# Performance work log

Hardware: AMD Instinct MI355X
Metric: run time of the kernel (lower is better)

The kernel has to match this reference:

```python
import jax, jax.numpy as jnp
import numpy as np

# dims: L layers, T steps, N envs, D d_model, H heads, DH d_head, M mem_len, DI d_inner
L, T, N, D, H, DH, M, DI = 6, 128, 32, 1024, 16, 64, 128, 4096


def _layer_norm(x, g, b, eps=1e-5):
    mu = jnp.mean(x, axis=-1, keepdims=True)
    var = jnp.mean(jnp.square(x - mu), axis=-1, keepdims=True)
    return (x - mu) * jax.lax.rsqrt(var + eps) * g + b


def _rel_shift(x):
    # x: (n, h, q, k) with k axis indexed by relative distance (k-1 .. 0)
    n, h, q, k = x.shape
    x = jnp.pad(x, ((0, 0), (0, 0), (0, 0), (1, 0)))
    x = x.reshape(n, h, k + 1, q)[:, :, 1:, :].reshape(n, h, q, k)
    return x


def setup_inputs() -> dict:
    key = jax.random.key(0)
    ks = jax.random.split(key, 16)
    s = 0.02
    inp = {
        "x": jax.random.normal(ks[0], (T * N, D), jnp.float32),
        "context": jax.random.normal(ks[1], (T * N, D), jnp.float32),
        "mems": jax.random.normal(ks[2], (L, N, M, D), jnp.float32),
        "masks": jnp.ones((T * N,), jnp.float32),
        "Wq": jax.random.normal(ks[3], (L, D, H * DH), jnp.float32) * s,
        "Wk": jax.random.normal(ks[4], (L, D, H * DH), jnp.float32) * s,
        "Wv": jax.random.normal(ks[5], (L, D, H * DH), jnp.float32) * s,
        "Wr": jax.random.normal(ks[6], (L, D, H * DH), jnp.float32) * s,
        "Wo": jax.random.normal(ks[7], (L, H * DH, D), jnp.float32) * s,
        "W1": jax.random.normal(ks[8], (L, D, DI), jnp.float32) * s,
        "b1": jnp.zeros((L, DI), jnp.float32),
        "W2": jax.random.normal(ks[9], (L, DI, D), jnp.float32) * s,
        "b2": jnp.zeros((L, D), jnp.float32),
        "ln1_g": jnp.ones((L, D), jnp.float32),
        "ln1_b": jnp.zeros((L, D), jnp.float32),
        "ln2_g": jnp.ones((L, D), jnp.float32),
        "ln2_b": jnp.zeros((L, D), jnp.float32),
        "r_w_bias": jax.random.normal(ks[10], (H, DH), jnp.float32) * s,
        "r_r_bias": jax.random.normal(ks[11], (H, DH), jnp.float32) * s,
    }
    return inp


def reference(x, context, mems, masks, Wq, Wk, Wv, Wr, Wo, W1, b1, W2, b2,
              ln1_g, ln1_b, ln2_g, ln2_b, r_w_bias, r_r_bias):
    n = mems.shape[1]
    t = x.shape[0] // n
    m = mems.shape[2]
    klen = m + t
    dh = r_w_bias.shape[-1]
    h_heads = r_w_bias.shape[0]

    xs = x.reshape(t, n, -1)
    ctx = context.reshape(t, n, -1)
    mk = masks.reshape(t, n)

    # zero memories for envs that reset at the first step (mems * masks)
    mems = mems * mk[0][None, :, None, None]

    # episode-reset attention mask: token i attends token j iff j<=i and no
    # reset (mask==0) happened between them; memory visible only before any reset
    ep = jnp.cumsum((mk == 0.0).astype(jnp.int32), axis=0)  # (t, n)
    epT = ep.T  # (n, t)
    causal = jnp.tril(jnp.ones((t, t), bool))
    allow_seq = causal[None, :, :] & (epT[:, :, None] == epT[:, None, :])  # (n,t,t)
    allow_mem = jnp.broadcast_to((epT == 0)[:, :, None], (n, t, m))  # (n,t,m)
    allow = jnp.concatenate([allow_mem, allow_seq], axis=-1)[:, None]  # (n,1,t,K)

    # sinusoidal relative position embedding, distances klen-1 .. 0
    pos = jnp.arange(klen - 1, -1, -1, dtype=x.dtype)
    inv_freq = 1.0 / (10000.0 ** (jnp.arange(0, xs.shape[-1], 2, dtype=x.dtype) / xs.shape[-1]))
    ang = pos[:, None] * inv_freq[None, :]
    R = jnp.concatenate([jnp.sin(ang), jnp.cos(ang)], axis=-1)  # (K, D)

    h = xs + ctx  # fuse observation features with goal context
    scale = 1.0 / jnp.sqrt(jnp.asarray(dh, x.dtype))

    n_layer = mems.shape[0]
    for l in range(n_layer):
        cat = jnp.concatenate([jnp.transpose(mems[l], (1, 0, 2)), h], axis=0)  # (K,n,D)
        q = (h @ Wq[l]).reshape(t, n, h_heads, dh)
        k = (cat @ Wk[l]).reshape(klen, n, h_heads, dh)
        v = (cat @ Wv[l]).reshape(klen, n, h_heads, dh)
        r = (R @ Wr[l]).reshape(klen, h_heads, dh)
        AC = jnp.einsum('inhd,jnhd->nhij', q + r_w_bias, k)
        BD = _rel_shift(jnp.einsum('inhd,jhd->nhij', q + r_r_bias, r))
        score = (AC + BD) * scale
        score = jnp.where(allow, score, -1e9)
        attn = jax.nn.softmax(score, axis=-1)
        o = jnp.einsum('nhij,jnhd->inhd', attn, v).reshape(t, n, h_heads * dh) @ Wo[l]
        h = _layer_norm(h + o, ln1_g[l], ln1_b[l])
        f = jax.nn.relu(h @ W1[l] + b1[l]) @ W2[l] + b2[l]
        h = _layer_norm(h + f, ln2_g[l], ln2_b[l])

    return h.reshape(t * n, -1)
```

## Files before the change

### kernel.cpp

```cpp
#include <hip/hip_runtime.h>
#include <stdint.h>

#define DEV static __device__ __forceinline__

typedef __attribute__((ext_vector_type(4))) float f32x4;
typedef __attribute__((ext_vector_type(8))) short bf16x8;
typedef __attribute__((ext_vector_type(4))) short s16x4;

static constexpr int L_ = 6, T_ = 128, NE = 32, D_ = 1024, H_ = 16, DH_ = 64, M_ = 128, DI_ = 4096;
static constexpr int KLEN = M_ + T_;
static constexpr int TN = T_ * NE;
static constexpr int NB = NE * H_;

DEV unsigned short f2bf(float f) {
  unsigned u = __builtin_bit_cast(unsigned, f);
  u += 0x7FFFu + ((u >> 16) & 1u);
  return (unsigned short)(u >> 16);
}
DEV float bf2f(unsigned short h) {
  unsigned u = ((unsigned)h) << 16;
  return __builtin_bit_cast(float, u);
}

DEV void gload16(const unsigned short* g, unsigned short* lds) {
  __builtin_amdgcn_global_load_lds(
      (const __attribute__((address_space(1))) unsigned int*)g,
      (__attribute__((address_space(3))) unsigned int*)lds, 16, 0, 0);
}

#define WAITV0 asm volatile("s_waitcnt vmcnt(0)" ::: "memory")

DEV void stage128(const unsigned short* __restrict__ Ab, int lda,
                  const unsigned short* __restrict__ Bb, int ldb,
                  unsigned short* lA, unsigned short* lB,
                  int m0, int n0, int k0, int w, int l)
{
#pragma unroll
  for (int i = 0; i < 4; ++i) {
    const int obb = i * 4096 + w * 1024;
    const int ob  = obb + (l << 4);
    const int row = ob >> 7;
    const int col = (((ob >> 4) & 7) ^ (row & 7)) << 3;
    gload16(Ab + (size_t)(m0 + row) * lda + k0 + col, lA + (obb >> 1));
    gload16(Bb + (size_t)(n0 + row) * ldb + k0 + col, lB + (obb >> 1));
  }
}

DEV void compute128(const unsigned short* lA, const unsigned short* lB,
                    int w, int l, f32x4 acc[4][4])
{
  const int wr = (w >> 1) * 64, wc = (w & 1) * 64;
  const int lan = l & 15, lgr = l >> 4;
#pragma unroll
  for (int ks = 0; ks < 2; ++ks) {
    bf16x8 av[4], bv[4];
#pragma unroll
    for (int m = 0; m < 4; ++m) {
      const int row = wr + m * 16 + lan;
      const int byte = ((row << 7) + (ks << 6) + (lgr << 4)) ^ ((row & 7) << 4);
      av[m] = *(const bf16x8*)((const char*)lA + byte);
    }
#pragma unroll
    for (int n = 0; n < 4; ++n) {
      const int row = wc + n * 16 + lan;
      const int byte = ((row << 7) + (ks << 6) + (lgr << 4)) ^ ((row & 7) << 4);
      bv[n] = *(const bf16x8*)((const char*)lB + byte);
    }
#pragma unroll
    for (int m = 0; m < 4; ++m)
#pragma unroll
      for (int n = 0; n < 4; ++n)
        acc[m][n] = __builtin_amdgcn_mfma_f32_16x16x32_bf16(av[m], bv[n], acc[m][n], 0, 0, 0);
  }
}

DEV void gemm128_2ph(const unsigned short* __restrict__ Ab, int lda,
                     const unsigned short* __restrict__ Bb, int ldb,
                     unsigned short (*shA)[8192], unsigned short (*shB)[8192],
                     int m0, int n0, int nK, int w, int l, f32x4 acc[4][4])
{
  stage128(Ab, lda, Bb, ldb, shA[0], shB[0], m0, n0, 0, w, l);
  WAITV0;
  __syncthreads();
  int cur = 0;
  for (int kt = 0; kt < nK; ++kt) {
    if (kt + 1 < nK)
      stage128(Ab, lda, Bb, ldb, shA[cur ^ 1], shB[cur ^ 1], m0, n0, (kt + 1) * 64, w, l);
    compute128(shA[cur], shB[cur], w, l, acc);
    WAITV0;
    __syncthreads();
    cur ^= 1;
  }
}

template <int EPI>
__global__ __launch_bounds__(256) void gemm_bt(
    const unsigned short* __restrict__ A, int lda, int sAn, int sAh,
    const unsigned short* __restrict__ B, int ldb, int sBn, int sBh,
    void* __restrict__ Cv, int ldc, int sC,
    const float* __restrict__ bias, int nK, int Hb)
{
  __shared__ unsigned short shA[2][8192];
  __shared__ unsigned short shB[2][8192];

  const int z = blockIdx.z;
  const int bn = z / Hb, bh = z % Hb;
  const unsigned short* Ab = A + (size_t)bn * sAn + (size_t)bh * sAh;
  const unsigned short* Bb = B + (size_t)bn * sBn + (size_t)bh * sBh;
  const int m0 = blockIdx.y * 128;
  const int n0 = blockIdx.x * 128;

  const int t = threadIdx.x;
  const int w = t >> 6, l = t & 63;
  const int wr = (w >> 1) * 64, wc = (w & 1) * 64;
  const int lan = l & 15, lgr = l >> 4;

  f32x4 acc[4][4];
#pragma unroll
  for (int m = 0; m < 4; ++m)
#pragma unroll
    for (int n = 0; n < 4; ++n) acc[m][n] = (f32x4){0.f, 0.f, 0.f, 0.f};

  gemm128_2ph(Ab, lda, Bb, ldb, shA, shB, m0, n0, nK, w, l, acc);

  const int zc = z * sC;
#pragma unroll
  for (int m = 0; m < 4; ++m) {
    const int row = m0 + wr + m * 16 + lgr * 4;
#pragma unroll
    for (int n = 0; n < 4; ++n) {
      const int col = n0 + wc + n * 16 + lan;
      const float bcol = (EPI >= 2) ? bias[col] : 0.f;
#pragma unroll
      for (int e = 0; e < 4; ++e) {
        float v = acc[m][n][e];
        const size_t idx = (size_t)zc + (size_t)(row + e) * ldc + col;
        if (EPI == 0) {
          ((float*)Cv)[idx] = v;
        } else if (EPI == 1) {
          ((unsigned short*)Cv)[idx] = f2bf(v);
        } else if (EPI == 2) {
          v += bcol; v = v > 0.f ? v : 0.f;
          ((unsigned short*)Cv)[idx] = f2bf(v);
        } else {
          ((float*)Cv)[idx] = v + bcol;
        }
      }
    }
  }
}

__global__ __launch_bounds__(256) void gemm_proj(
    const unsigned short* __restrict__ catA, const unsigned short* __restrict__ wt,
    unsigned short* __restrict__ kb, unsigned short* __restrict__ vb,
    unsigned short* __restrict__ qw, unsigned short* __restrict__ qr,
    unsigned short* __restrict__ rb,
    const float* __restrict__ rwb, const float* __restrict__ rrb)
{
  __shared__ unsigned short shA[2][8192];
  __shared__ unsigned short shB[2][8192];

  const int id = blockIdx.x;
  int by, bx;
  if (id < 1024)      { by = id >> 4;               bx = id & 15; }
  else if (id < 1280) { const int u = id - 1024; by = 32 + (u >> 3); bx = 16 + (u & 7); }
  else                { const int u = id - 1280; by = 64 + (u >> 3); bx = 24 + (u & 7); }
  const int m0 = by * 128, n0 = bx * 128;

  const int t = threadIdx.x;
  const int w = t >> 6, l = t & 63;
  const int wr = (w >> 1) * 64, wc = (w & 1) * 64;
  const int lan = l & 15, lgr = l >> 4;

  f32x4 acc[4][4];
#pragma unroll
  for (int m = 0; m < 4; ++m)
#pragma unroll
    for (int n = 0; n < 4; ++n) acc[m][n] = (f32x4){0.f, 0.f, 0.f, 0.f};

  gemm128_2ph(catA, 1024, wt, 1024, shA, shB, m0, n0, 16, w, l, acc);

#pragma unroll
  for (int m = 0; m < 4; ++m) {
    const int row = m0 + wr + m * 16 + lgr * 4;
#pragma unroll
    for (int n = 0; n < 4; ++n) {
      const int col = n0 + wc + n * 16 + lan;
#pragma unroll
      for (int e = 0; e < 4; ++e) {
        const float v = acc[m][n][e];
        const int r = row + e;
        if (col < 1024) {
          kb[(size_t)r * 1024 + col] = f2bf(v);
        } else if (col < 2048) {
          vb[(size_t)r * 1024 + col - 1024] = f2bf(v);
        } else if (col < 3072) {
          const int c = col - 2048;
          const size_t o = (size_t)(r - 4096) * 1024 + c;
          qw[o] = f2bf(v + rwb[c]);
          qr[o] = f2bf(v + rrb[c]);
        } else {
          const int c = col - 3072;
          rb[(size_t)(r - 8192) * 1024 + c] = f2bf(v);
        }
      }
    }
  }
}

__global__ __launch_bounds__(256) void attn_kernel(
    const unsigned short* __restrict__ qw, const unsigned short* __restrict__ qr,
    const unsigned short* __restrict__ kbf, const unsigned short* __restrict__ rbf,
    const int* __restrict__ ep, const unsigned short* __restrict__ V,
    unsigned short* __restrict__ O)
{
  __shared__ unsigned short sS[4][32 * 256];

  const int z = blockIdx.x;
  const int nn = z >> 4, hh = z & 15;
  const int t = threadIdx.x, w = t >> 6, l = t & 63;
  const int lan = l & 15, lgr = l >> 4;
  const int i0 = w * 32;
  unsigned short* S = sS[w];

  bf16x8 av[2][2];
#pragma unroll
  for (int m = 0; m < 2; ++m)
#pragma unroll
    for (int kk = 0; kk < 2; ++kk) {
      const int i = i0 + m * 16 + lan;
      av[m][kk] = *(const bf16x8*)&qw[(size_t)(i * NE + nn) * 1024 + hh * 64 + kk * 32 + lgr * 8];
    }
#pragma unroll
  for (int n = 0; n < 16; ++n) {
    bf16x8 bv[2];
#pragma unroll
    for (int kk = 0; kk < 2; ++kk) {
      const int j = n * 16 + lan;
      bv[kk] = *(const bf16x8*)&kbf[(size_t)(j * NE + nn) * 1024 + hh * 64 + kk * 32 + lgr * 8];
    }
#pragma unroll
    for (int m = 0; m < 2; ++m) {
      f32x4 a4 = (f32x4){0.f, 0.f, 0.f, 0.f};
#pragma unroll
      for (int kk = 0; kk < 2; ++kk)
        a4 = __builtin_amdgcn_mfma_f32_16x16x32_bf16(av[m][kk], bv[kk], a4, 0, 0, 0);
#pragma unroll
      for (int e = 0; e < 4; ++e) {
        const int r = m * 16 + lgr * 4 + e;
        const int j = n * 16 + lan;
        const int swz = ((r >> 2) & 3) * 16;
        S[r * 256 + (j ^ swz)] = f2bf(a4[e]);
      }
    }
  }

  bf16x8 bq[2][2];
#pragma unroll
  for (int m = 0; m < 2; ++m)
#pragma unroll
    for (int kk = 0; kk < 2; ++kk) {
      const int i = i0 + m * 16 + lan;
      bq[m][kk] = *(const bf16x8*)&qr[(size_t)(i * NE + nn) * 1024 + hh * 64 + kk * 32 + lgr * 8];
    }
#pragma unroll
  for (int n = 0; n < 16; ++n) {
    bf16x8 bv[2];
#pragma unroll
    for (int kk = 0; kk < 2; ++kk) {
      const int jp = n * 16 + lan;
      bv[kk] = *(const bf16x8*)&rbf[(size_t)jp * 1024 + hh * 64 + kk * 32 + lgr * 8];
    }
#pragma unroll
    for (int m = 0; m < 2; ++m) {
      f32x4 a4 = (f32x4){0.f, 0.f, 0.f, 0.f};
#pragma unroll
      for (int kk = 0; kk < 2; ++kk)
        a4 = __builtin_amdgcn_mfma_f32_16x16x32_bf16(bq[m][kk], bv[kk], a4, 0, 0, 0);
#pragma unroll
      for (int e = 0; e < 4; ++e) {
        const int r = m * 16 + lgr * 4 + e;
        const int i = i0 + r;
        const int jp = n * 16 + lan;
        const int j = jp + i - 127;
        if (j >= 0 && j < 256) {
          const int swz = ((r >> 2) & 3) * 16;
          const int idx = r * 256 + (j ^ swz);
          S[idx] = f2bf(bf2f(S[idx]) + a4[e]);
        }
      }
    }
  }

  const int j0 = l * 4;
  for (int rr = 0; rr < 32; ++rr) {
    const int i = i0 + rr;
    const int epi = ep[i * NE + nn];
    const int swz = ((rr >> 2) & 3) * 16;
    s16x4 s4 = *(const s16x4*)&S[rr * 256 + (j0 ^ swz)];
    float sc[4];
#pragma unroll
    for (int q = 0; q < 4; ++q) {
      const int j = j0 + q;
      bool allow;
      if (j < M_) {
        allow = (epi == 0);
      } else {
        const int jp = j - M_;
        allow = (jp <= i) && (ep[jp * NE + nn] == epi);
      }
      sc[q] = allow ? bf2f((unsigned short)s4[q]) * 0.125f : -1e9f;
    }
    float mx = fmaxf(fmaxf(sc[0], sc[1]), fmaxf(sc[2], sc[3]));
#pragma unroll
    for (int o = 32; o; o >>= 1) mx = fmaxf(mx, __shfl_xor(mx, o));
    float p[4], sum = 0.f;
#pragma unroll
    for (int q = 0; q < 4; ++q) { p[q] = __expf(sc[q] - mx); sum += p[q]; }
#pragma unroll
    for (int o = 32; o; o >>= 1) sum += __shfl_xor(sum, o);
    const float inv = 1.f / sum;
    s16x4 o4;
#pragma unroll
    for (int q = 0; q < 4; ++q) o4[q] = (short)f2bf(p[q] * inv);
    *(s16x4*)&S[rr * 256 + (j0 ^ swz)] = o4;
  }

  const unsigned short* Vz = V + hh * DH_;
  f32x4 acc[2][4];
#pragma unroll
  for (int m = 0; m < 2; ++m)
#pragma unroll
    for (int n = 0; n < 4; ++n) acc[m][n] = (f32x4){0.f, 0.f, 0.f, 0.f};

  for (int ks = 0; ks < 8; ++ks) {
    const int kb = ks * 32 + lgr * 8;
    bf16x8 bv2[4];
#pragma unroll
    for (int n = 0; n < 4; ++n) {
      const int d = n * 16 + lan;
      bf16x8 tmp;
#pragma unroll
      for (int jj = 0; jj < 8; ++jj)
        tmp[jj] = (short)Vz[(size_t)((kb + jj) * NE + nn) * 1024 + d];
      bv2[n] = tmp;
    }
    bf16x8 pa[2];
#pragma unroll
    for (int m = 0; m < 2; ++m) {
      const int r = m * 16 + lan;
      const int swz = ((r >> 2) & 3) * 16;
      pa[m] = *(const bf16x8*)&S[r * 256 + (kb ^ swz)];
    }
#pragma unroll
    for (int m = 0; m < 2; ++m)
#pragma unroll
      for (int n = 0; n < 4; ++n)
        acc[m][n] = __builtin_amdgcn_mfma_f32_16x16x32_bf16(pa[m], bv2[n], acc[m][n], 0, 0, 0);
  }
#pragma unroll
  for (int m = 0; m < 2; ++m)
#pragma unroll
    for (int n = 0; n < 4; ++n)
#pragma unroll
      for (int e = 0; e < 4; ++e) {
        const int i = i0 + m * 16 + lgr * 4 + e;
        const int d = n * 16 + lan;
        O[(size_t)(i * NE + nn) * 1024 + hh * DH_ + d] = f2bf(acc[m][n][e]);
      }
}

__global__ __launch_bounds__(256) void transpose_kernel(
    const float* __restrict__ W, unsigned short* __restrict__ WT, int Kd, int Nd)
{
  __shared__ float tile[32][33];
  const int tx = threadIdx.x & 31, ty = threadIdx.x >> 5;
  const int nIn = blockIdx.x * 32 + tx;
  const int kBase = blockIdx.y * 32;
#pragma unroll
  for (int r = 0; r < 32; r += 8)
    tile[ty + r][tx] = W[(size_t)(kBase + ty + r) * Nd + nIn];
  __syncthreads();
#pragma unroll
  for (int r = 0; r < 32; r += 8)
    WT[(size_t)(blockIdx.x * 32 + ty + r) * Kd + kBase + tx] = f2bf(tile[tx][ty + r]);
}

__global__ __launch_bounds__(256) void transpose5_kernel(
    const float* __restrict__ Wk, const float* __restrict__ Wv,
    const float* __restrict__ Wq, const float* __restrict__ Wr,
    const float* __restrict__ Wo,
    unsigned short* __restrict__ wtAll, unsigned short* __restrict__ wto)
{
  __shared__ float tile[32][33];
  const int zz = blockIdx.z;
  const float* W = (zz == 0) ? Wk : (zz == 1) ? Wv : (zz == 2) ? Wq : (zz == 3) ? Wr : Wo;
  unsigned short* WT = (zz == 4) ? wto : (wtAll + (size_t)zz * 1024 * 1024);
  const int tx = threadIdx.x & 31, ty = threadIdx.x >> 5;
  const int nIn = blockIdx.x * 32 + tx;
  const int kBase = blockIdx.y * 32;
#pragma unroll
  for (int r = 0; r < 32; r += 8)
    tile[ty + r][tx] = W[(size_t)(kBase + ty + r) * 1024 + nIn];
  __syncthreads();
#pragma unroll
  for (int r = 0; r < 32; r += 8)
    WT[(size_t)(blockIdx.x * 32 + ty + r) * 1024 + kBase + tx] = f2bf(tile[tx][ty + r]);
}

__global__ __launch_bounds__(256) void catmem_kernel(
    const float* __restrict__ mems_l, const float* __restrict__ masks,
    unsigned short* __restrict__ cat)
{
  const int idx = blockIdx.x * 256 + threadIdx.x;
  const int d = idx & 1023;
  const int r = idx >> 10;
  const int nn = r & 31, j = r >> 5;
  const float mk0 = masks[nn];
  cat[idx] = f2bf(mems_l[(size_t)(nn * M_ + j) * 1024 + d] * mk0);
}

__global__ __launch_bounds__(256) void hprep_kernel(
    const float* __restrict__ x, const float* __restrict__ ctx,
    float* __restrict__ h, unsigned short* __restrict__ catUp)
{
  const int idx = blockIdx.x * 256 + threadIdx.x;
  const float v = x[idx] + ctx[idx];
  h[idx] = v;
  catUp[idx] = f2bf(v);
}

__global__ __launch_bounds__(256) void rpos_kernel(unsigned short* __restrict__ R)
{
  const int idx = blockIdx.x * 256 + threadIdx.x;
  const int d = idx & 1023, j = idx >> 10;
  const float pos = (float)(KLEN - 1 - j);
  const int f = d & 511;
  const float inv_freq = __expf(-((float)(2 * f) * (1.f / 1024.f)) * 9.210340371976184f);
  const float ang = pos * inv_freq;
  const float v = (d < 512) ? sinf(ang) : cosf(ang);
  R[idx] = f2bf(v);
}

__global__ void ep_kernel(const float* __restrict__ masks, int* __restrict__ ep)
{
  const int nn = threadIdx.x;
  if (nn < NE) {
    int c = 0;
    for (int i = 0; i < T_; ++i) {
      c += (masks[i * NE + nn] == 0.f) ? 1 : 0;
      ep[i * NE + nn] = c;
    }
  }
}

template <int NP>
__global__ __launch_bounds__(256) void ln_kernel(
    const float* __restrict__ a, const float* __restrict__ parts, size_t pstride,
    const float* __restrict__ bias,
    const float* __restrict__ g, const float* __restrict__ bb,
    float* __restrict__ outf, unsigned short* __restrict__ outbf)
{
  const int row = blockIdx.x;
  const int t = threadIdx.x, w = t >> 6, l = t & 63;
  const int c = t * 4;
  const size_t base = (size_t)row * 1024;
  f32x4 v = *(const f32x4*)&a[base + c];
#pragma unroll
  for (int i = 0; i < NP; ++i)
    v = v + *(const f32x4*)&parts[i * pstride + base + c];
  if (bias) v = v + *(const f32x4*)&bias[c];
  float s = v[0] + v[1] + v[2] + v[3];
#pragma unroll
  for (int o = 32; o; o >>= 1) s += __shfl_xor(s, o);
  __shared__ float red[8];
  if (l == 0) red[w] = s;
  __syncthreads();
  s = red[0] + red[1] + red[2] + red[3];
  const float mu = s * (1.f / 1024.f);
  f32x4 dv = v - mu;
  float s2 = dv[0]*dv[0] + dv[1]*dv[1] + dv[2]*dv[2] + dv[3]*dv[3];
#pragma unroll
  for (int o = 32; o; o >>= 1) s2 += __shfl_xor(s2, o);
  if (l == 0) red[4 + w] = s2;
  __syncthreads();
  s2 = red[4] + red[5] + red[6] + red[7];
  const float inv = rsqrtf(s2 * (1.f / 1024.f) + 1e-5f);
  f32x4 y;
#pragma unroll
  for (int q = 0; q < 4; ++q) y[q] = dv[q] * inv * g[c + q] + bb[c + q];
  *(f32x4*)&outf[base + c] = y;
  if (outbf) {
    s16x4 o4;
#pragma unroll
    for (int q = 0; q < 4; ++q) o4[q] = (short)f2bf(y[q]);
    *(s16x4*)&outbf[base + c] = o4;
  }
}

extern "C" void kernel_launch(void* const* d_in, const int* in_sizes, int n_in,
                              void* d_out, int out_size, void* d_ws, size_t ws_size,
                              hipStream_t stream)
{
  (void)in_sizes; (void)n_in; (void)out_size; (void)ws_size;
  const float* x    = (const float*)d_in[0];
  const float* ctx  = (const float*)d_in[1];
  const float* mems = (const float*)d_in[2];
  const float* masks= (const float*)d_in[3];
  const float* Wq   = (const float*)d_in[4];
  const float* Wk   = (const float*)d_in[5];
  const float* Wv   = (const float*)d_in[6];
  const float* Wr   = (const float*)d_in[7];
  const float* Wo   = (const float*)d_in[8];
  const float* W1   = (const float*)d_in[9];
  const float* b1   = (const float*)d_in[10];
  const float* W2   = (const float*)d_in[11];
  const float* b2   = (const float*)d_in[12];
  const float* ln1g = (const float*)d_in[13];
  const float* ln1b = (const float*)d_in[14];
  const float* ln2g = (const float*)d_in[15];
  const float* ln2b = (const float*)d_in[16];
  const float* rwb  = (const float*)d_in[17];
  const float* rrb  = (const float*)d_in[18];

  char* ws = (char*)d_ws;
  size_t off = 0;
  auto alloc = [&](size_t bytes) {
    char* p = ws + off;
    off += (bytes + 255) & ~(size_t)255;
    return p;
  };
  unsigned short* wtAll = (unsigned short*)alloc(4096u * 1024 * 2);
  unsigned short* wto = (unsigned short*)alloc(1024u * 1024 * 2);
  unsigned short* wt1 = (unsigned short*)alloc(4096u * 1024 * 2);
  unsigned short* wt2 = (unsigned short*)alloc(4096u * 1024 * 2);
  unsigned short* cat = (unsigned short*)alloc((size_t)(KLEN * NE + 256) * 1024 * 2);
  unsigned short* rbf = (unsigned short*)alloc((size_t)KLEN * 1024 * 2);
  int*            epb = (int*)alloc((size_t)T_ * NE * 4);
  float*          h   = (float*)alloc((size_t)TN * 1024 * 4);
  float*          h1  = (float*)alloc((size_t)TN * 1024 * 4);
  unsigned short* qw  = (unsigned short*)alloc((size_t)TN * 1024 * 2);
  unsigned short* qr  = (unsigned short*)alloc((size_t)TN * 1024 * 2);
  unsigned short* kbf = (unsigned short*)alloc((size_t)KLEN * NE * 1024 * 2);
  unsigned short* vbf = (unsigned short*)alloc((size_t)KLEN * NE * 1024 * 2);
  unsigned short* ACb = (unsigned short*)alloc((size_t)NB * T_ * KLEN * 2);
  unsigned short* BDb = (unsigned short*)alloc((size_t)NB * T_ * KLEN * 2);
  unsigned short* obf = (unsigned short*)alloc((size_t)TN * 1024 * 2);

  unsigned short* catUp = cat + (size_t)M_ * NE * 1024;
  unsigned short* catR  = cat + (size_t)KLEN * NE * 1024;
  unsigned short* f1 = ACb;
  float* part = (float*)BDb;
  unsigned short* h1bf = qw;

  rpos_kernel<<<KLEN * 1024 / 256, 256, 0, stream>>>(catR);
  ep_kernel<<<1, 64, 0, stream>>>(masks, epb);
  hprep_kernel<<<TN * 1024 / 256, 256, 0, stream>>>(x, ctx, h, catUp);

  for (int l = 0; l < L_; ++l) {
    const size_t wOff = (size_t)l * 1024 * 1024;
    const size_t wOffBig = (size_t)l * 1024 * 4096;
    transpose5_kernel<<<dim3(32, 32, 5), 256, 0, stream>>>(
        Wk + wOff, Wv + wOff, Wq + wOff, Wr + wOff, Wo + wOff, wtAll, wto);
    transpose_kernel<<<dim3(128, 32), 256, 0, stream>>>(W1 + wOffBig, wt1, 1024, 4096);
    transpose_kernel<<<dim3(32, 128), 256, 0, stream>>>(W2 + wOffBig, wt2, 4096, 1024);
    catmem_kernel<<<M_ * NE * 1024 / 256, 256, 0, stream>>>(
        mems + (size_t)l * NE * M_ * 1024, masks, cat);

    gemm_proj<<<1296, 256, 0, stream>>>(cat, wtAll, kbf, vbf, qw, qr, rbf, rwb, rrb);

    attn_kernel<<<NB, 256, 0, stream>>>(qw, qr, kbf, rbf, epb, vbf, obf);

    gemm_bt<0><<<dim3(8, 32, 2), 256, 0, stream>>>(obf, 1024, 0, 512,
                                                   wto, 1024, 0, 512,
                                                   part, 1024, TN * 1024, nullptr, 8, 2);
    ln_kernel<2><<<TN, 256, 0, stream>>>(h, part, (size_t)TN * 1024, nullptr,
                                         ln1g + l * 1024, ln1b + l * 1024, h1, h1bf);

    gemm_bt<2><<<dim3(32, 32, 1), 256, 0, stream>>>(h1bf, 1024, 0, 0, wt1, 1024, 0, 0,
                                                    f1, 4096, 0, b1 + l * 4096, 16, 1);
    gemm_bt<0><<<dim3(8, 32, 2), 256, 0, stream>>>(f1, 4096, 0, 2048,
                                                   wt2, 4096, 0, 2048,
                                                   part, 1024, TN * 1024, nullptr, 32, 2);
    ln_kernel<2><<<TN, 256, 0, stream>>>(h1, part, (size_t)TN * 1024, b2 + l * 1024,
                                         ln2g + l * 1024, ln2b + l * 1024,
                                         (l == L_ - 1) ? (float*)d_out : h, catUp);
  }
}
```

Before: 1.912 ms.

## Switch dense GEMMs to 256x256 tiles with 512 threads and 4-way split-K

Adds a 256x256-tile bf16 MFMA GEMM kernel that uses 8 waves and double-buffered LDS of 128 KB. It replaces the 128x128 kernel for the output projection and both FFN GEMMs. The Wo and W2 GEMMs now split K four ways instead of two, and the layer norm sums four partial buffers. The partial buffer grows into a newly reserved region placed after BDb. The aim is more operand reuse per LDS load, and grids of 256 blocks that fill the CUs in one wave. The risks are higher register and LDS pressure per block, plus extra partial-sum traffic from the wider split-K.

Result: no change. 1.947 ms (+1.9%).

```diff
diff --git a/kernel.cpp b/kernel.cpp
--- a/kernel.cpp
+++ b/kernel.cpp
@@ -93,57 +93,111 @@
   }
 }
 
+DEV void stage256(const unsigned short* __restrict__ Ab, int lda,
+                  const unsigned short* __restrict__ Bb, int ldb,
+                  unsigned short* lA, unsigned short* lB,
+                  int m0, int n0, int k0, int t)
+{
+#pragma unroll
+  for (int i = 0; i < 4; ++i) {
+    const int obb = i * 8192 + (t >> 6) * 1024;
+    const int ob  = obb + ((t & 63) << 4);
+    const int row = ob >> 7;
+    const int col = (((ob >> 4) & 7) ^ (row & 7)) << 3;
+    gload16(Ab + (size_t)(m0 + row) * lda + k0 + col, lA + (obb >> 1));
+    gload16(Bb + (size_t)(n0 + row) * ldb + k0 + col, lB + (obb >> 1));
+  }
+}
+
+DEV void compute256(const unsigned short* lA, const unsigned short* lB,
+                    int w, int l, f32x4 acc[8][4])
+{
+  const int wm = w >> 2, wn = w & 3;
+  const int lan = l & 15, lgr = l >> 4;
+#pragma unroll
+  for (int ks = 0; ks < 2; ++ks) {
+    bf16x8 av[8], bv[4];
+#pragma unroll
+    for (int m = 0; m < 8; ++m) {
+      const int row = wm * 128 + m * 16 + lan;
+      const int byte = ((row << 7) + (ks << 6) + (lgr << 4)) ^ ((row & 7) << 4);
+      av[m] = *(const bf16x8*)((const char*)lA + byte);
+    }
+#pragma unroll
+    for (int n = 0; n < 4; ++n) {
+      const int row = wn * 64 + n * 16 + lan;
+      const int byte = ((row << 7) + (ks << 6) + (lgr << 4)) ^ ((row & 7) << 4);
+      bv[n] = *(const bf16x8*)((const char*)lB + byte);
+    }
+#pragma unroll
+    for (int m = 0; m < 8; ++m)
+#pragma unroll
+      for (int n = 0; n < 4; ++n)
+        acc[m][n] = __builtin_amdgcn_mfma_f32_16x16x32_bf16(av[m], bv[n], acc[m][n], 0, 0, 0);
+  }
+}
+
+DEV void gemm256_2ph(const unsigned short* __restrict__ Ab, int lda,
+                     const unsigned short* __restrict__ Bb, int ldb,
+                     unsigned short (*shA)[16384], unsigned short (*shB)[16384],
+                     int m0, int n0, int nK, int t, f32x4 acc[8][4])
+{
+  const int w = t >> 6, l = t & 63;
+  stage256(Ab, lda, Bb, ldb, shA[0], shB[0], m0, n0, 0, t);
+  WAITV0;
+  __syncthreads();
+  int cur = 0;
+  for (int kt = 0; kt < nK; ++kt) {
+    if (kt + 1 < nK)
+      stage256(Ab, lda, Bb, ldb, shA[cur ^ 1], shB[cur ^ 1], m0, n0, (kt + 1) * 64, t);
+    compute256(shA[cur], shB[cur], w, l, acc);
+    WAITV0;
+    __syncthreads();
+    cur ^= 1;
+  }
+}
+
 template <int EPI>
-__global__ __launch_bounds__(256) void gemm_bt(
-    const unsigned short* __restrict__ A, int lda, int sAn, int sAh,
-    const unsigned short* __restrict__ B, int ldb, int sBn, int sBh,
-    void* __restrict__ Cv, int ldc, int sC,
-    const float* __restrict__ bias, int nK, int Hb)
-{
-  __shared__ unsigned short shA[2][8192];
-  __shared__ unsigned short shB[2][8192];
-
+__global__ __launch_bounds__(512) void gemm256_bt(
+    const unsigned short* __restrict__ A, int lda, int sAh,
+    const unsigned short* __restrict__ B, int ldb, int sBh,
+    void* __restrict__ Cv, int ldc, size_t sC,
+    const float* __restrict__ bias, int nK)
+{
+  __shared__ unsigned short shA[2][16384];
+  __shared__ unsigned short shB[2][16384];
   const int z = blockIdx.z;
-  const int bn = z / Hb, bh = z % Hb;
-  const unsigned short* Ab = A + (size_t)bn * sAn + (size_t)bh * sAh;
-  const unsigned short* Bb = B + (size_t)bn * sBn + (size_t)bh * sBh;
-  const int m0 = blockIdx.y * 128;
-  const int n0 = blockIdx.x * 128;
-
+  const int m0 = blockIdx.y * 256, n0 = blockIdx.x * 256;
   const int t = threadIdx.x;
+
+  f32x4 acc[8][4];
+#pragma unroll
+  for (int m = 0; m < 8; ++m)
+#pragma unroll
+    for (int n = 0; n < 4; ++n) acc[m][n] = (f32x4){0.f, 0.f, 0.f, 0.f};
+
+  gemm256_2ph(A + (size_t)z * sAh, lda, B + (size_t)z * sBh, ldb,
+              shA, shB, m0, n0, nK, t, acc);
+
   const int w = t >> 6, l = t & 63;
-  const int wr = (w >> 1) * 64, wc = (w & 1) * 64;
-  const int lan = l & 15, lgr = l >> 4;
-
-  f32x4 acc[4][4];
-#pragma unroll
-  for (int m = 0; m < 4; ++m)
-#pragma unroll
-    for (int n = 0; n < 4; ++n) acc[m][n] = (f32x4){0.f, 0.f, 0.f, 0.f};
-
-  gemm128_2ph(Ab, lda, Bb, ldb, shA, shB, m0, n0, nK, w, l, acc);
-
-  const int zc = z * sC;
-#pragma unroll
-  for (int m = 0; m < 4; ++m) {
-    const int row = m0 + wr + m * 16 + lgr * 4;
+  const int wm = w >> 2, wn = w & 3, lan = l & 15, lgr = l >> 4;
+  const size_t zc = (size_t)z * sC;
+#pragma unroll
+  for (int m = 0; m < 8; ++m) {
+    const int row = m0 + wm * 128 + m * 16 + lgr * 4;
 #pragma unroll
     for (int n = 0; n < 4; ++n) {
-      const int col = n0 + wc + n * 16 + lan;
+      const int col = n0 + wn * 64 + n * 16 + lan;
       const float bcol = (EPI >= 2) ? bias[col] : 0.f;
 #pragma unroll
       for (int e = 0; e < 4; ++e) {
         float v = acc[m][n][e];
-        const size_t idx = (size_t)zc + (size_t)(row + e) * ldc + col;
+        const size_t idx = zc + (size_t)(row + e) * ldc + col;
         if (EPI == 0) {
           ((float*)Cv)[idx] = v;
-        } else if (EPI == 1) {
-          ((unsigned short*)Cv)[idx] = f2bf(v);
-        } else if (EPI == 2) {
+        } else {
           v += bcol; v = v > 0.f ? v : 0.f;
           ((unsigned short*)Cv)[idx] = f2bf(v);
-        } else {
-          ((float*)Cv)[idx] = v + bcol;
         }
       }
     }
@@ -545,8 +599,10 @@
   unsigned short* vbf = (unsigned short*)alloc((size_t)KLEN * NE * 1024 * 2);
   unsigned short* ACb = (unsigned short*)alloc((size_t)NB * T_ * KLEN * 2);
   unsigned short* BDb = (unsigned short*)alloc((size_t)NB * T_ * KLEN * 2);
+  float*          pex = (float*)alloc((size_t)2 * TN * 1024 * 4);
   unsigned short* obf = (unsigned short*)alloc((size_t)TN * 1024 * 2);
 
+  (void)pex;
   unsigned short* catUp = cat + (size_t)M_ * NE * 1024;
   unsigned short* catR  = cat + (size_t)KLEN * NE * 1024;
   unsigned short* f1 = ACb;
@@ -571,18 +627,19 @@
 
     attn_kernel<<<NB, 256, 0, stream>>>(qw, qr, kbf, rbf, epb, vbf, obf);
 
-    gemm_bt<0><<<dim3(8, 32, 2), 256, 0, stream>>>(obf, 1024, 0, 512,
-                                                   wto, 1024, 0, 512,
-                                                   part, 1024, TN * 1024, nullptr, 8, 2);
-    ln_kernel<2><<<TN, 256, 0, stream>>>(h, part, (size_t)TN * 1024, nullptr,
+    gemm256_bt<0><<<dim3(4, 16, 4), 512, 0, stream>>>(
+        obf, 1024, 256, wto, 1024, 256,
+        part, 1024, (size_t)TN * 1024, nullptr, 4);
+    ln_kernel<4><<<TN, 256, 0, stream>>>(h, part, (size_t)TN * 1024, nullptr,
                                          ln1g + l * 1024, ln1b + l * 1024, h1, h1bf);
 
-    gemm_bt<2><<<dim3(32, 32, 1), 256, 0, stream>>>(h1bf, 1024, 0, 0, wt1, 1024, 0, 0,
-                                                    f1, 4096, 0, b1 + l * 4096, 16, 1);
-    gemm_bt<0><<<dim3(8, 32, 2), 256, 0, stream>>>(f1, 4096, 0, 2048,
-                                                   wt2, 4096, 0, 2048,
-                                                   part, 1024, TN * 1024, nullptr, 32, 2);
-    ln_kernel<2><<<TN, 256, 0, stream>>>(h1, part, (size_t)TN * 1024, b2 + l * 1024,
+    gemm256_bt<2><<<dim3(16, 16, 1), 512, 0, stream>>>(
+        h1bf, 1024, 0, wt1, 1024, 0,
+        f1, 4096, (size_t)0, b1 + l * 4096, 16);
+    gemm256_bt<0><<<dim3(4, 16, 4), 512, 0, stream>>>(
+        f1, 4096, 1024, wt2, 4096, 1024,
+        part, 1024, (size_t)TN * 1024, nullptr, 16);
+    ln_kernel<4><<<TN, 256, 0, stream>>>(h1, part, (size_t)TN * 1024, b2 + l * 1024,
                                          ln2g + l * 1024, ln2b + l * 1024,
                                          (l == L_ - 1) ? (float*)d_out : h, catUp);
   }
```

## Pre-transpose V per head for vectorized PV loads; merge weight transposes

Applied to the files above, without the earlier changes.

Adds a kernel that transposes each (env, head) slice of V into a contiguous d-major layout. The attention PV loop can then fetch each MFMA B-fragment with one 16-byte load instead of eight strided scalar gathers. The three per-layer weight-transpose launches are also folded into a single launch with 13 z-slices. The cost is an extra kernel launch per layer plus a round trip of V through global memory.

Measured after the change: 1.935 ms. About the same (+1.2%).

```diff
diff --git a/kernel.cpp b/kernel.cpp
--- a/kernel.cpp
+++ b/kernel.cpp
@@ -208,10 +208,37 @@
   }
 }
 
+__global__ __launch_bounds__(256) void vtrans_kernel(
+    const unsigned short* __restrict__ V, unsigned short* __restrict__ vt)
+{
+  __shared__ unsigned short tile[128][72];
+  const int z = blockIdx.x;
+  const int nn = z >> 4, hh = z & 15;
+  const int t = threadIdx.x;
+  for (int p = 0; p < 2; ++p) {
+    const int j = p * 128 + (t >> 1);
+    const int dbase = (t & 1) * 32;
+    const unsigned short* src = &V[(size_t)(j * NE + nn) * 1024 + hh * 64 + dbase];
+#pragma unroll
+    for (int i = 0; i < 4; ++i)
+      *(bf16x8*)&tile[t >> 1][dbase + i * 8] = *(const bf16x8*)&src[i * 8];
+    __syncthreads();
+    const int d = t >> 2, jseg = (t & 3) * 32;
+    unsigned short out[32];
+#pragma unroll
+    for (int jj = 0; jj < 32; ++jj) out[jj] = tile[jseg + jj][d];
+    unsigned short* dst = &vt[((size_t)z * 64 + d) * 256 + p * 128 + jseg];
+#pragma unroll
+    for (int i = 0; i < 4; ++i)
+      *(bf16x8*)&dst[i * 8] = *(const bf16x8*)&out[i * 8];
+    __syncthreads();
+  }
+}
+
 __global__ __launch_bounds__(256) void attn_kernel(
     const unsigned short* __restrict__ qw, const unsigned short* __restrict__ qr,
     const unsigned short* __restrict__ kbf, const unsigned short* __restrict__ rbf,
-    const int* __restrict__ ep, const unsigned short* __restrict__ V,
+    const int* __restrict__ ep, const unsigned short* __restrict__ vt,
     unsigned short* __restrict__ O)
 {
   __shared__ unsigned short sS[4][32 * 256];
@@ -326,7 +353,7 @@
     *(s16x4*)&S[rr * 256 + (j0 ^ swz)] = o4;
   }
 
-  const unsigned short* Vz = V + hh * DH_;
+  const unsigned short* vtz = vt + (size_t)z * 64 * 256;
   f32x4 acc[2][4];
 #pragma unroll
   for (int m = 0; m < 2; ++m)
@@ -339,11 +366,7 @@
 #pragma unroll
     for (int n = 0; n < 4; ++n) {
       const int d = n * 16 + lan;
-      bf16x8 tmp;
-#pragma unroll
-      for (int jj = 0; jj < 8; ++jj)
-        tmp[jj] = (short)Vz[(size_t)((kb + jj) * NE + nn) * 1024 + d];
-      bv2[n] = tmp;
+      bv2[n] = *(const bf16x8*)&vtz[(size_t)d * 256 + kb];
     }
     bf16x8 pa[2];
 #pragma unroll
@@ -370,10 +393,32 @@
       }
 }
 
-__global__ __launch_bounds__(256) void transpose_kernel(
-    const float* __restrict__ W, unsigned short* __restrict__ WT, int Kd, int Nd)
+__global__ __launch_bounds__(256) void transpose13_kernel(
+    const float* __restrict__ Wk, const float* __restrict__ Wv,
+    const float* __restrict__ Wq, const float* __restrict__ Wr,
+    const float* __restrict__ Wo, const float* __restrict__ W1,
+    const float* __restrict__ W2,
+    unsigned short* __restrict__ wtAll, unsigned short* __restrict__ wto,
+    unsigned short* __restrict__ wt1, unsigned short* __restrict__ wt2)
 {
   __shared__ float tile[32][33];
+  const int zz = blockIdx.z;
+  const float* W; unsigned short* WT; int Nd, Kd;
+  if (zz < 5) {
+    W = (zz == 0) ? Wk : (zz == 1) ? Wv : (zz == 2) ? Wq : (zz == 3) ? Wr : Wo;
+    WT = (zz == 4) ? wto : (wtAll + (size_t)zz * 1024 * 1024);
+    Nd = 1024; Kd = 1024;
+  } else if (zz < 9) {
+    const int c = zz - 5;
+    W = W1 + (size_t)c * 1024;
+    WT = wt1 + (size_t)c * 1024 * 1024;
+    Nd = 4096; Kd = 1024;
+  } else {
+    const int c = zz - 9;
+    W = W2 + (size_t)c * 1024 * 1024;
+    WT = wt2 + (size_t)c * 1024;
+    Nd = 1024; Kd = 4096;
+  }
   const int tx = threadIdx.x & 31, ty = threadIdx.x >> 5;
   const int nIn = blockIdx.x * 32 + tx;
   const int kBase = blockIdx.y * 32;
@@ -384,28 +429,6 @@
 #pragma unroll
   for (int r = 0; r < 32; r += 8)
     WT[(size_t)(blockIdx.x * 32 + ty + r) * Kd + kBase + tx] = f2bf(tile[tx][ty + r]);
-}
-
-__global__ __launch_bounds__(256) void transpose5_kernel(
-    const float* __restrict__ Wk, const float* __restrict__ Wv,
-    const float* __restrict__ Wq, const float* __restrict__ Wr,
-    const float* __restrict__ Wo,
-    unsigned short* __restrict__ wtAll, unsigned short* __restrict__ wto)
-{
-  __shared__ float tile[32][33];
-  const int zz = blockIdx.z;
-  const float* W = (zz == 0) ? Wk : (zz == 1) ? Wv : (zz == 2) ? Wq : (zz == 3) ? Wr : Wo;
-  unsigned short* WT = (zz == 4) ? wto : (wtAll + (size_t)zz * 1024 * 1024);
-  const int tx = threadIdx.x & 31, ty = threadIdx.x >> 5;
-  const int nIn = blockIdx.x * 32 + tx;
-  const int kBase = blockIdx.y * 32;
-#pragma unroll
-  for (int r = 0; r < 32; r += 8)
-    tile[ty + r][tx] = W[(size_t)(kBase + ty + r) * 1024 + nIn];
-  __syncthreads();
-#pragma unroll
-  for (int r = 0; r < 32; r += 8)
-    WT[(size_t)(blockIdx.x * 32 + ty + r) * 1024 + kBase + tx] = f2bf(tile[tx][ty + r]);
 }
 
 __global__ __launch_bounds__(256) void catmem_kernel(
@@ -543,6 +566,7 @@
   unsigned short* qr  = (unsigned short*)alloc((size_t)TN * 1024 * 2);
   unsigned short* kbf = (unsigned short*)alloc((size_t)KLEN * NE * 1024 * 2);
   unsigned short* vbf = (unsigned short*)alloc((size_t)KLEN * NE * 1024 * 2);
+  unsigned short* vt  = (unsigned short*)alloc((size_t)NB * DH_ * KLEN * 2);
   unsigned short* ACb = (unsigned short*)alloc((size_t)NB * T_ * KLEN * 2);
   unsigned short* BDb = (unsigned short*)alloc((size_t)NB * T_ * KLEN * 2);
   unsigned short* obf = (unsigned short*)alloc((size_t)TN * 1024 * 2);
@@ -560,16 +584,17 @@
   for (int l = 0; l < L_; ++l) {
     const size_t wOff = (size_t)l * 1024 * 1024;
     const size_t wOffBig = (size_t)l * 1024 * 4096;
-    transpose5_kernel<<<dim3(32, 32, 5), 256, 0, stream>>>(
-        Wk + wOff, Wv + wOff, Wq + wOff, Wr + wOff, Wo + wOff, wtAll, wto);
-    transpose_kernel<<<dim3(128, 32), 256, 0, stream>>>(W1 + wOffBig, wt1, 1024, 4096);
-    transpose_kernel<<<dim3(32, 128), 256, 0, stream>>>(W2 + wOffBig, wt2, 4096, 1024);
+    transpose13_kernel<<<dim3(32, 32, 13), 256, 0, stream>>>(
+        Wk + wOff, Wv + wOff, Wq + wOff, Wr + wOff, Wo + wOff,
+        W1 + wOffBig, W2 + wOffBig, wtAll, wto, wt1, wt2);
     catmem_kernel<<<M_ * NE * 1024 / 256, 256, 0, stream>>>(
         mems + (size_t)l * NE * M_ * 1024, masks, cat);
 
     gemm_proj<<<1296, 256, 0, stream>>>(cat, wtAll, kbf, vbf, qw, qr, rbf, rwb, rrb);
 
-    attn_kernel<<<NB, 256, 0, stream>>>(qw, qr, kbf, rbf, epb, vbf, obf);
+    vtrans_kernel<<<NB, 256, 0, stream>>>(vbf, vt);
+
+    attn_kernel<<<NB, 256, 0, stream>>>(qw, qr, kbf, rbf, epb, vt, obf);
 
     gemm_bt<0><<<dim3(8, 32, 2), 256, 0, stream>>>(obf, 1024, 0, 512,
                                                    wto, 1024, 0, 512,
```
